# Performance work log

Measured on AMD Instinct MI355X. Metric: run time of the kernel, lower is better.

The kernel has to match this reference:

```python
import jax, jax.numpy as jnp
import numpy as np

B, L = 1024, 4096        # cycles x timesteps
CC = 3                   # SC channels (SC[...,2:3] = nominal capacity)
XC = 2 + CC              # p_net input: [SOC, T, SC...]
# bounds from params['a123'] for (R_1, 1/R_1C_1, OCV-U, -M_H, K_H)
LB = jnp.array([0.005, 0.025, 0.1, 0.0, 0.002], dtype=jnp.float32)
UB = jnp.array([0.02, 0.07, 1.0, 0.055, 0.025], dtype=jnp.float32)


def setup_inputs() -> dict:
    key = jax.random.key(0)
    ks = jax.random.split(key, 10)
    t = jnp.broadcast_to(jnp.arange(L, dtype=jnp.float32), (B, L))  # monotone time
    I = 1.0 + 0.1 * jax.random.normal(ks[0], (B, L))  # current, bounded away from 0 (IR_estim divides by I)
    T = jax.random.normal(ks[1], (B, L))              # temperature
    dummy = jax.random.normal(ks[2], (B, L))          # unused column 3
    SOC = jax.random.uniform(ks[3], (B, L))
    X = jnp.stack([t, I, T, dummy, SOC], axis=-1)     # [B, L, 5]
    SC = jax.random.uniform(ks[4], (B, CC), minval=0.5, maxval=1.5)
    std = 0.1  # init_network_weights: normal(0, 0.1), zero bias
    pW1 = std * jax.random.normal(ks[5], (XC, 2 * XC))
    pb1 = jnp.zeros((2 * XC,), jnp.float32)
    pW2 = std * jax.random.normal(ks[6], (2 * XC, 5))
    pb2 = jnp.zeros((5,), jnp.float32)
    rW1 = std * jax.random.normal(ks[7], (XC, 1))
    rb1 = jnp.zeros((1,), jnp.float32)
    rW2 = std * jax.random.normal(ks[8], (1, 1))
    rb2 = jnp.zeros((1,), jnp.float32)
    return dict(X=X, SC=SC, pW1=pW1, pb1=pb1, pW2=pW2, pb2=pb2,
                rW1=rW1, rb1=rb1, rW2=rW2, rb2=rb2)


def reference(X, SC, pW1, pb1, pW2, pb2, rW1, rb1, rW2, rb2):
    t = X[..., 0:1]
    I = X[..., 1:2]
    T = X[..., 2:3]
    SOC = X[..., 4:]
    sc_b = jnp.broadcast_to(SC[:, None, :], (X.shape[0], X.shape[1], SC.shape[-1]))
    x = jnp.concatenate([SOC, T, sc_b], axis=-1)                 # [B, L, XC]
    p = jax.nn.softplus(x @ pW1 + pb1) @ pW2 + pb2               # [B, L, 5]
    theta = LB + (UB - LB) * jax.nn.sigmoid(0.01 * p)
    R_1 = theta[..., 0:1]
    RC_r = theta[..., 1:2]
    OCV_U = theta[..., 2:3]
    M_Hn = theta[..., 3:4]   # -M_H
    K_H = theta[..., 4:5]
    r = jax.nn.softplus(x[:, 0, :] @ rW1 + rb1) @ rW2 + rb2      # [B, 1]
    R_s_init = SC[..., 2:3] * (1.0 + r)
    U_H0 = jnp.zeros((X.shape[0], 1), X.dtype)
    U_10 = -OCV_U[:, 0, :] - U_H0 - I[:, 0, :] * R_s_init
    y0 = jnp.concatenate([U_H0, U_10], axis=-1)                  # [B, 2]

    dt = jnp.swapaxes(t[:, 1:, :] - t[:, :-1, :], 0, 1)          # [L-1, B, 1]
    tm = lambda a: jnp.swapaxes(a[:, :-1, :], 0, 1)              # step inputs use X_ode[:, i]
    scan_in = (dt, tm(I), tm(R_1), tm(RC_r), tm(M_Hn), tm(K_H))

    def step(y, inp):  # explicit Euler, IRODEFunc derivative
        dt_i, I_i, R1_i, RC_i, MH_i, KH_i = inp
        U_H = y[..., 0:1]
        U_1 = y[..., 1:2]
        dU_H = -KH_i * I_i * (-MH_i - U_H)
        dU_1 = RC_i * (R1_i * I_i - U_1)
        y = y + dt_i * jnp.concatenate([dU_H, dU_1], axis=-1)
        return y, y

    _, ys = jax.lax.scan(step, y0, scan_in)                      # [L-1, B, 2]
    voltages = jnp.concatenate([y0[None], ys], axis=0)           # [L, B, 2]
    voltages = jnp.swapaxes(voltages, 0, 1)                      # [B, L, 2]
    U_H = voltages[..., 0:1]
    U_1 = voltages[..., 1:2]
    IR_estim = jnp.nanmean((-OCV_U - U_H - U_1) / I, axis=-2)    # [B, 1]
    return IR_estim
```

## Files before the change

kernel.cpp:

```cpp
#include <hip/hip_runtime.h>

#define NB   1024
#define NL   4096
#define TPB  256
#define QSTEP 1024
#define SPT  4

#define WS_PART 16640

typedef float v2f __attribute__((ext_vector_type(2)));

__device__ __forceinline__ float fast_rcp(float x) { return __builtin_amdgcn_rcpf(x); }
__device__ __forceinline__ float fexp2(float x) { return __builtin_amdgcn_exp2f(x); }
__device__ __forceinline__ float flog2(float x) { return __builtin_amdgcn_logf(x); }

#define L2E 1.44269504088896340736f
#define LN2 0.69314718055994530942f

#define SP_C0 1.0f
#define SP_C1 0.0864667f
#define SP_C2 (-0.0015685f)
#define SP_C3 2.5763e-5f

__global__ void __launch_bounds__(TPB) onenet_main(
    const float* __restrict__ X,   const float* __restrict__ SC,
    const float* __restrict__ pW1, const float* __restrict__ pb1,
    const float* __restrict__ pW2, const float* __restrict__ pb2,
    const float* __restrict__ rW1, const float* __restrict__ rb1,
    const float* __restrict__ rW2, const float* __restrict__ rb2,
    float* __restrict__ ws)
{
    __shared__ float4 tile[TPB * 5];
    __shared__ float  red[TPB / 64][9];

    const int bid  = blockIdx.x;
    const int row  = bid >> 2;
    const int q    = bid & 3;
    const int tid  = threadIdx.x;
    const int lane = tid & 63;
    const int w    = tid >> 6;

    const float* Xq = X + ((size_t)row * NL + (size_t)q * QSTEP) * 5;
    {
        const float4* gq = (const float4*)Xq;
#pragma unroll
        for (int k = 0; k < 5; ++k) {
            int widx = tid + TPB * k;
            int sw   = widx ^ ((widx >> 3) & 7);
            tile[sw] = gq[widx];
        }
    }

    const float sc0 = SC[row * 3 + 0];
    const float sc1 = SC[row * 3 + 1];
    const float sc2 = SC[row * 3 + 2];

    float W1S[10], W1T[10], BASE[10];
    float VR1[10], VRC[10], VOC[10], VMH[10], VKH[10];
#pragma unroll
    for (int j = 0; j < 10; ++j) {
        W1S[j]  = L2E * pW1[j];
        W1T[j]  = L2E * pW1[10 + j];
        BASE[j] = L2E * fmaf(sc0, pW1[20 + j],
                        fmaf(sc1, pW1[30 + j],
                        fmaf(sc2, pW1[40 + j], pb1[j])));
    }
    const float UBLB0 = 0.015f, UBLB1 = 0.045f, UBLB2 = 0.9f,
                UBLB3 = 0.055f, UBLB4 = 0.023f;
    const float KC = LN2 * 0.0025f;
#pragma unroll
    for (int j = 0; j < 10; ++j) {
        VR1[j] = KC * UBLB0 * pW2[5 * j + 0];
        VRC[j] = KC * UBLB1 * pW2[5 * j + 1];
        VOC[j] = KC * UBLB2 * pW2[5 * j + 2];
        VMH[j] = KC * UBLB3 * pW2[5 * j + 3];
        VKH[j] = KC * UBLB4 * pW2[5 * j + 4];
    }
    const float A0 = 0.005f + UBLB0 * fmaf(0.0025f, pb2[0], 0.5f);
    const float A1 = 0.025f + UBLB1 * fmaf(0.0025f, pb2[1], 0.5f);
    const float A2 = 0.1f   + UBLB2 * fmaf(0.0025f, pb2[2], 0.5f);
    const float A3 = 0.0f   + UBLB3 * fmaf(0.0025f, pb2[3], 0.5f);
    const float A4 = 0.002f + UBLB4 * fmaf(0.0025f, pb2[4], 0.5f);

    float Rs = 0.f;
    if (q == 0) {
        const float* x0 = X + (size_t)row * NL * 5;
        float T0 = x0[2], SOC0 = x0[4];
        float u = rb1[0];
        u = fmaf(SOC0, rW1[0], u);
        u = fmaf(T0,   rW1[1], u);
        u = fmaf(sc0,  rW1[2], u);
        u = fmaf(sc1,  rW1[3], u);
        u = fmaf(sc2,  rW1[4], u);
        float sp = LN2 * flog2(1.0f + fexp2(L2E * u));
        Rs = sc2 * (1.0f + fmaf(sp, rW2[0], rb2[0]));
    }

    __syncthreads();

    float f[20];
#pragma unroll
    for (int j = 0; j < 5; ++j) {
        int widx = 5 * tid + j;
        int sw   = widx ^ ((widx >> 3) & 7);
        *(float4*)&f[4 * j] = tile[sw];
    }
    float tn;
    {
        int wn  = 5 * ((tid + 1) & (TPB - 1));
        int swn = wn ^ ((wn >> 3) & 7);
        float tl = tile[swn].x;
        if (tid < TPB - 1)      tn = tl;
        else if (q == 3)        tn = f[15];
        else                    tn = Xq[QSTEP * 5];
    }

    v2f a = {1.f, 1.f}, b = {0.f, 0.f}, cS = {0.f, 0.f}, dS = {0.f, 0.f};
    v2f oaccv = {0.f, 0.f};
    float OCV0 = 0.f, I0 = 0.f;

#pragma unroll
    for (int ip = 0; ip < 2; ++ip) {
        const int i0 = 2 * ip, i1 = 2 * ip + 1;
        v2f SSv = { f[5 * i0 + 4], f[5 * i1 + 4] };
        v2f Ttv = { f[5 * i0 + 2], f[5 * i1 + 2] };
        v2f Iv  = { f[5 * i0 + 1], f[5 * i1 + 1] };
        float tnx1 = (i1 < SPT - 1) ? f[5 * i1 + 5] : tn;
        v2f dtv = { f[5 * i1 + 0] - f[5 * i0 + 0], tnx1 - f[5 * i1 + 0] };
        v2f invv = { fast_rcp(Iv.x), fast_rcp(Iv.y) };

        v2f tR1 = {A0, A0}, tRC = {A1, A1}, tOC = {A2, A2},
            tMH = {A3, A3}, tKH = {A4, A4};
#pragma unroll
        for (int j = 0; j < 10; ++j) {
            v2f pre = SSv * W1S[j] + Ttv * W1T[j] + BASE[j];
            v2f s   = pre * pre;
            v2f p   = s * SP_C3 + SP_C2;
            p = s * p + SP_C1;
            p = s * p + SP_C0;
            v2f lam = pre * 0.5f + p;
            tR1 += lam * VR1[j];
            tRC += lam * VRC[j];
            tOC += lam * VOC[j];
            tMH += lam * VMH[j];
            tKH += lam * VKH[j];
        }
        oaccv += tOC * invv;
        if (ip == 0) { OCV0 = tOC.x; I0 = Iv.x; }

        v2f g  = dtv * tKH * Iv;
        v2f hh = dtv * tRC;
        v2f bx = g * tMH;
        v2f by = hh * tR1 * Iv;

        {
            v2f sv = {1.f + g.x, 1.f - hh.x};
            v2f bv = {bx.x, by.x};
            v2f iv = {invv.x, invv.x};
            cS = iv * a + cS;
            dS = iv * b + dS;
            b  = sv * b + bv;
            a  = sv * a;
        }
        {
            v2f sv = {1.f + g.y, 1.f - hh.y};
            v2f bv = {bx.y, by.y};
            v2f iv = {invv.y, invv.y};
            cS = iv * a + cS;
            dS = iv * b + dS;
            b  = sv * b + bv;
            a  = sv * a;
        }
    }
    float oacc = -(oaccv.x + oaccv.y);

#pragma unroll
    for (int off = 1; off < 64; off <<= 1) {
        v2f a2, b2, c2, d2;
        a2.x = __shfl_down(a.x, off);  a2.y = __shfl_down(a.y, off);
        b2.x = __shfl_down(b.x, off);  b2.y = __shfl_down(b.y, off);
        c2.x = __shfl_down(cS.x, off); c2.y = __shfl_down(cS.y, off);
        d2.x = __shfl_down(dS.x, off); d2.y = __shfl_down(dS.y, off);
        float o2 = __shfl_down(oacc, off);
        v2f nb = a2 * b + b2;
        v2f nc = c2 * a + cS;
        v2f nd = (dS + d2) + c2 * b;
        a = a2 * a; b = nb; cS = nc; dS = nd;
        oacc += o2;
    }

    if (lane == 0) {
        red[w][0] = a.x;  red[w][1] = a.y;
        red[w][2] = b.x;  red[w][3] = b.y;
        red[w][4] = cS.x; red[w][5] = cS.y;
        red[w][6] = dS.x; red[w][7] = dS.y;
        red[w][8] = oacc;
    }
    __syncthreads();

    if (tid == 0) {
#pragma unroll
        for (int k = 1; k < TPB / 64; ++k) {
            v2f ak, bk, ck, dk;
            ak.x = red[k][0]; ak.y = red[k][1];
            bk.x = red[k][2]; bk.y = red[k][3];
            ck.x = red[k][4]; ck.y = red[k][5];
            dk.x = red[k][6]; dk.y = red[k][7];
            v2f nb = ak * b + bk;
            v2f nc = ck * a + cS;
            v2f nd = (dS + dk) + ck * b;
            a = ak * a; b = nb; cS = nc; dS = nd;
            oacc += red[k][8];
        }
        float* pw = ws + WS_PART + (size_t)bid * 12;
        pw[0] = a.x;  pw[1] = b.x;  pw[2] = cS.x; pw[3] = dS.x;
        pw[4] = a.y;  pw[5] = b.y;  pw[6] = cS.y; pw[7] = dS.y;
        pw[8] = oacc;
        if (q == 0) { pw[9] = OCV0; pw[10] = I0; pw[11] = Rs; }
    }
}

__global__ void __launch_bounds__(256) onenet_final(
    const float* __restrict__ ws, float* __restrict__ out)
{
    const int row = blockIdx.x * 256 + threadIdx.x;
    if (row >= NB) return;
    const float* p0 = ws + WS_PART + (size_t)row * 48;

    v2f a, b, cS, dS;
    a.x  = p0[0]; a.y  = p0[4];
    b.x  = p0[1]; b.y  = p0[5];
    cS.x = p0[2]; cS.y = p0[6];
    dS.x = p0[3]; dS.y = p0[7];
    float O = p0[8];
    float OCV0 = p0[9], I0 = p0[10], Rs = p0[11];
#pragma unroll
    for (int k = 1; k < 4; ++k) {
        const float* pk = p0 + k * 12;
        v2f ak, bk, ck, dk;
        ak.x = pk[0]; ak.y = pk[4];
        bk.x = pk[1]; bk.y = pk[5];
        ck.x = pk[2]; ck.y = pk[6];
        dk.x = pk[3]; dk.y = pk[7];
        v2f nb = ak * b + bk;
        v2f nc = ck * a + cS;
        v2f nd = (dS + dk) + ck * b;
        a = ak * a; b = nb; cS = nc; dS = nd;
        O += pk[8];
    }
    float U10 = -OCV0 - I0 * Rs;
    float SH  = dS.x;
    float S1  = fmaf(cS.y, U10, dS.y);
    out[row] = (O - SH - S1) * (1.0f / 4096.0f);
}

extern "C" void kernel_launch(void* const* d_in, const int* in_sizes, int n_in,
                              void* d_out, int out_size, void* d_ws, size_t ws_size,
                              hipStream_t stream) {
    const float* X   = (const float*)d_in[0];
    const float* SC  = (const float*)d_in[1];
    const float* pW1 = (const float*)d_in[2];
    const float* pb1 = (const float*)d_in[3];
    const float* pW2 = (const float*)d_in[4];
    const float* pb2 = (const float*)d_in[5];
    const float* rW1 = (const float*)d_in[6];
    const float* rb1 = (const float*)d_in[7];
    const float* rW2 = (const float*)d_in[8];
    const float* rb2 = (const float*)d_in[9];
    float* out = (float*)d_out;
    float* ws  = (float*)d_ws;

    onenet_main<<<NB * 4, TPB, 0, stream>>>(X, SC, pW1, pb1, pW2, pb2,
                                            rW1, rb1, rW2, rb2, ws);
    onenet_final<<<NB / 256, 256, 0, stream>>>(ws, out);
}
```

Baseline: 141.7 us.

## Fuse main and final kernels with one block per row and direct-to-LDS loads

Each row is now handled by a single 256-thread block that processes 16 timesteps per thread in four chunks. This removes the second reduction kernel and the workspace round-trip. The full 80 KB row tile is loaded with global_load_lds straight into shared memory, replacing the register-staged loads. The large LDS footprint cuts occupancy to about one block per CU, and the grid shrinks from 4096 blocks to 1024, which limits latency hiding.

```diff
diff --git a/kernel.cpp b/kernel.cpp
--- a/kernel.cpp
+++ b/kernel.cpp
@@ -3,10 +3,7 @@
 #define NB   1024
 #define NL   4096
 #define TPB  256
-#define QSTEP 1024
-#define SPT  4
-
-#define WS_PART 16640
+#define NCH  4
 
 typedef float v2f __attribute__((ext_vector_type(2)));
 
@@ -22,33 +19,32 @@
 #define SP_C2 (-0.0015685f)
 #define SP_C3 2.5763e-5f
 
-__global__ void __launch_bounds__(TPB) onenet_main(
+__global__ void __launch_bounds__(TPB) onenet_fused(
     const float* __restrict__ X,   const float* __restrict__ SC,
     const float* __restrict__ pW1, const float* __restrict__ pb1,
     const float* __restrict__ pW2, const float* __restrict__ pb2,
     const float* __restrict__ rW1, const float* __restrict__ rb1,
     const float* __restrict__ rW2, const float* __restrict__ rb2,
-    float* __restrict__ ws)
+    float* __restrict__ out)
 {
-    __shared__ float4 tile[TPB * 5];
-    __shared__ float  red[TPB / 64][9];
-
-    const int bid  = blockIdx.x;
-    const int row  = bid >> 2;
-    const int q    = bid & 3;
+    __shared__ float4 tile[5120];
+
+    const int row  = blockIdx.x;
     const int tid  = threadIdx.x;
     const int lane = tid & 63;
     const int w    = tid >> 6;
 
-    const float* Xq = X + ((size_t)row * NL + (size_t)q * QSTEP) * 5;
-    {
-        const float4* gq = (const float4*)Xq;
-#pragma unroll
-        for (int k = 0; k < 5; ++k) {
-            int widx = tid + TPB * k;
-            int sw   = widx ^ ((widx >> 3) & 7);
-            tile[sw] = gq[widx];
-        }
+    const float* Xrow = X + (size_t)row * NL * 5;
+
+#pragma unroll
+    for (int k = 0; k < 20; ++k) {
+        int jbase = 256 * k + 64 * w;
+        int j     = jbase + lane;
+        int sj    = j ^ ((j >> 3) & 7);
+        __builtin_amdgcn_global_load_lds(
+            (const __attribute__((address_space(1))) void*)(Xrow + 4 * (size_t)sj),
+            (__attribute__((address_space(3))) void*)&tile[jbase],
+            16, 0, 0);
     }
 
     const float sc0 = SC[row * 3 + 0];
@@ -82,10 +78,9 @@
     const float A3 = 0.0f   + UBLB3 * fmaf(0.0025f, pb2[3], 0.5f);
     const float A4 = 0.002f + UBLB4 * fmaf(0.0025f, pb2[4], 0.5f);
 
-    float Rs = 0.f;
-    if (q == 0) {
-        const float* x0 = X + (size_t)row * NL * 5;
-        float T0 = x0[2], SOC0 = x0[4];
+    float Rs;
+    {
+        float T0 = Xrow[2], SOC0 = Xrow[4];
         float u = rb1[0];
         u = fmaf(SOC0, rW1[0], u);
         u = fmaf(T0,   rW1[1], u);
@@ -98,78 +93,83 @@
 
     __syncthreads();
 
-    float f[20];
-#pragma unroll
-    for (int j = 0; j < 5; ++j) {
-        int widx = 5 * tid + j;
-        int sw   = widx ^ ((widx >> 3) & 7);
-        *(float4*)&f[4 * j] = tile[sw];
-    }
-    float tn;
-    {
-        int wn  = 5 * ((tid + 1) & (TPB - 1));
-        int swn = wn ^ ((wn >> 3) & 7);
-        float tl = tile[swn].x;
-        if (tid < TPB - 1)      tn = tl;
-        else if (q == 3)        tn = f[15];
-        else                    tn = Xq[QSTEP * 5];
-    }
-
     v2f a = {1.f, 1.f}, b = {0.f, 0.f}, cS = {0.f, 0.f}, dS = {0.f, 0.f};
     v2f oaccv = {0.f, 0.f};
     float OCV0 = 0.f, I0 = 0.f;
-
-#pragma unroll
-    for (int ip = 0; ip < 2; ++ip) {
-        const int i0 = 2 * ip, i1 = 2 * ip + 1;
-        v2f SSv = { f[5 * i0 + 4], f[5 * i1 + 4] };
-        v2f Ttv = { f[5 * i0 + 2], f[5 * i1 + 2] };
-        v2f Iv  = { f[5 * i0 + 1], f[5 * i1 + 1] };
-        float tnx1 = (i1 < SPT - 1) ? f[5 * i1 + 5] : tn;
-        v2f dtv = { f[5 * i1 + 0] - f[5 * i0 + 0], tnx1 - f[5 * i1 + 0] };
-        v2f invv = { fast_rcp(Iv.x), fast_rcp(Iv.y) };
-
-        v2f tR1 = {A0, A0}, tRC = {A1, A1}, tOC = {A2, A2},
-            tMH = {A3, A3}, tKH = {A4, A4};
-#pragma unroll
-        for (int j = 0; j < 10; ++j) {
-            v2f pre = SSv * W1S[j] + Ttv * W1T[j] + BASE[j];
-            v2f s   = pre * pre;
-            v2f p   = s * SP_C3 + SP_C2;
-            p = s * p + SP_C1;
-            p = s * p + SP_C0;
-            v2f lam = pre * 0.5f + p;
-            tR1 += lam * VR1[j];
-            tRC += lam * VRC[j];
-            tOC += lam * VOC[j];
-            tMH += lam * VMH[j];
-            tKH += lam * VKH[j];
-        }
-        oaccv += tOC * invv;
-        if (ip == 0) { OCV0 = tOC.x; I0 = Iv.x; }
-
-        v2f g  = dtv * tKH * Iv;
-        v2f hh = dtv * tRC;
-        v2f bx = g * tMH;
-        v2f by = hh * tR1 * Iv;
-
+    const float* tf = (const float*)tile;
+
+#pragma unroll
+    for (int c = 0; c < NCH; ++c) {
+        float f[20];
+#pragma unroll
+        for (int jj = 0; jj < 5; ++jj) {
+            int i4 = 20 * tid + 5 * c + jj;
+            int s4 = i4 ^ ((i4 >> 3) & 7);
+            *(float4*)&f[4 * jj] = tile[s4];
+        }
+        float tn;
         {
-            v2f sv = {1.f + g.x, 1.f - hh.x};
-            v2f bv = {bx.x, by.x};
-            v2f iv = {invv.x, invv.x};
-            cS = iv * a + cS;
-            dS = iv * b + dS;
-            b  = sv * b + bv;
-            a  = sv * a;
-        }
-        {
-            v2f sv = {1.f + g.y, 1.f - hh.y};
-            v2f bv = {bx.y, by.y};
-            v2f iv = {invv.y, invv.y};
-            cS = iv * a + cS;
-            dS = iv * b + dS;
-            b  = sv * b + bv;
-            a  = sv * a;
+            int i4 = 20 * tid + 5 * c + 5;
+            if (i4 < 5120) {
+                int s4 = i4 ^ ((i4 >> 3) & 7);
+                tn = tf[4 * s4];
+            } else {
+                tn = f[15];
+            }
+        }
+
+#pragma unroll
+        for (int ip = 0; ip < 2; ++ip) {
+            const int i0 = 2 * ip, i1 = 2 * ip + 1;
+            v2f SSv = { f[5 * i0 + 4], f[5 * i1 + 4] };
+            v2f Ttv = { f[5 * i0 + 2], f[5 * i1 + 2] };
+            v2f Iv  = { f[5 * i0 + 1], f[5 * i1 + 1] };
+            float tnx1 = (ip == 0) ? f[5 * i1 + 5] : tn;
+            v2f dtv = { f[5 * i1 + 0] - f[5 * i0 + 0], tnx1 - f[5 * i1 + 0] };
+            v2f invv = { fast_rcp(Iv.x), fast_rcp(Iv.y) };
+
+            v2f tR1 = {A0, A0}, tRC = {A1, A1}, tOC = {A2, A2},
+                tMH = {A3, A3}, tKH = {A4, A4};
+#pragma unroll
+            for (int j = 0; j < 10; ++j) {
+                v2f pre = SSv * W1S[j] + Ttv * W1T[j] + BASE[j];
+                v2f s   = pre * pre;
+                v2f p   = s * SP_C3 + SP_C2;
+                p = s * p + SP_C1;
+                p = s * p + SP_C0;
+                v2f lam = pre * 0.5f + p;
+                tR1 += lam * VR1[j];
+                tRC += lam * VRC[j];
+                tOC += lam * VOC[j];
+                tMH += lam * VMH[j];
+                tKH += lam * VKH[j];
+            }
+            oaccv += tOC * invv;
+            if (c == 0 && ip == 0) { OCV0 = tOC.x; I0 = Iv.x; }
+
+            v2f g  = dtv * tKH * Iv;
+            v2f hh = dtv * tRC;
+            v2f bx = g * tMH;
+            v2f by = hh * tR1 * Iv;
+
+            {
+                v2f sv = {1.f + g.x, 1.f - hh.x};
+                v2f bv = {bx.x, by.x};
+                v2f iv = {invv.x, invv.x};
+                cS = iv * a + cS;
+                dS = iv * b + dS;
+                b  = sv * b + bv;
+                a  = sv * a;
+            }
+            {
+                v2f sv = {1.f + g.y, 1.f - hh.y};
+                v2f bv = {bx.y, by.y};
+                v2f iv = {invv.y, invv.y};
+                cS = iv * a + cS;
+                dS = iv * b + dS;
+                b  = sv * b + bv;
+                a  = sv * a;
+            }
         }
     }
     float oacc = -(oaccv.x + oaccv.y);
@@ -189,12 +189,14 @@
         oacc += o2;
     }
 
+    __syncthreads();
+    float* redf = (float*)tile;
     if (lane == 0) {
-        red[w][0] = a.x;  red[w][1] = a.y;
-        red[w][2] = b.x;  red[w][3] = b.y;
-        red[w][4] = cS.x; red[w][5] = cS.y;
-        red[w][6] = dS.x; red[w][7] = dS.y;
-        red[w][8] = oacc;
+        redf[w * 12 + 0] = a.x;  redf[w * 12 + 1] = a.y;
+        redf[w * 12 + 2] = b.x;  redf[w * 12 + 3] = b.y;
+        redf[w * 12 + 4] = cS.x; redf[w * 12 + 5] = cS.y;
+        redf[w * 12 + 6] = dS.x; redf[w * 12 + 7] = dS.y;
+        redf[w * 12 + 8] = oacc;
     }
     __syncthreads();
 
@@ -202,56 +204,21 @@
 #pragma unroll
         for (int k = 1; k < TPB / 64; ++k) {
             v2f ak, bk, ck, dk;
-            ak.x = red[k][0]; ak.y = red[k][1];
-            bk.x = red[k][2]; bk.y = red[k][3];
-            ck.x = red[k][4]; ck.y = red[k][5];
-            dk.x = red[k][6]; dk.y = red[k][7];
+            ak.x = redf[k * 12 + 0]; ak.y = redf[k * 12 + 1];
+            bk.x = redf[k * 12 + 2]; bk.y = redf[k * 12 + 3];
+            ck.x = redf[k * 12 + 4]; ck.y = redf[k * 12 + 5];
+            dk.x = redf[k * 12 + 6]; dk.y = redf[k * 12 + 7];
             v2f nb = ak * b + bk;
             v2f nc = ck * a + cS;
             v2f nd = (dS + dk) + ck * b;
             a = ak * a; b = nb; cS = nc; dS = nd;
-            oacc += red[k][8];
-        }
-        float* pw = ws + WS_PART + (size_t)bid * 12;
-        pw[0] = a.x;  pw[1] = b.x;  pw[2] = cS.x; pw[3] = dS.x;
-        pw[4] = a.y;  pw[5] = b.y;  pw[6] = cS.y; pw[7] = dS.y;
-        pw[8] = oacc;
-        if (q == 0) { pw[9] = OCV0; pw[10] = I0; pw[11] = Rs; }
-    }
-}
-
-__global__ void __launch_bounds__(256) onenet_final(
-    const float* __restrict__ ws, float* __restrict__ out)
-{
-    const int row = blockIdx.x * 256 + threadIdx.x;
-    if (row >= NB) return;
-    const float* p0 = ws + WS_PART + (size_t)row * 48;
-
-    v2f a, b, cS, dS;
-    a.x  = p0[0]; a.y  = p0[4];
-    b.x  = p0[1]; b.y  = p0[5];
-    cS.x = p0[2]; cS.y = p0[6];
-    dS.x = p0[3]; dS.y = p0[7];
-    float O = p0[8];
-    float OCV0 = p0[9], I0 = p0[10], Rs = p0[11];
-#pragma unroll
-    for (int k = 1; k < 4; ++k) {
-        const float* pk = p0 + k * 12;
-        v2f ak, bk, ck, dk;
-        ak.x = pk[0]; ak.y = pk[4];
-        bk.x = pk[1]; bk.y = pk[5];
-        ck.x = pk[2]; ck.y = pk[6];
-        dk.x = pk[3]; dk.y = pk[7];
-        v2f nb = ak * b + bk;
-        v2f nc = ck * a + cS;
-        v2f nd = (dS + dk) + ck * b;
-        a = ak * a; b = nb; cS = nc; dS = nd;
-        O += pk[8];
-    }
-    float U10 = -OCV0 - I0 * Rs;
-    float SH  = dS.x;
-    float S1  = fmaf(cS.y, U10, dS.y);
-    out[row] = (O - SH - S1) * (1.0f / 4096.0f);
+            oacc += redf[k * 12 + 8];
+        }
+        float U10 = -OCV0 - I0 * Rs;
+        float SH  = dS.x;
+        float S1  = fmaf(cS.y, U10, dS.y);
+        out[row] = (oacc - SH - S1) * (1.0f / 4096.0f);
+    }
 }
 
 extern "C" void kernel_launch(void* const* d_in, const int* in_sizes, int n_in,
@@ -268,9 +235,8 @@
     const float* rW2 = (const float*)d_in[8];
     const float* rb2 = (const float*)d_in[9];
     float* out = (float*)d_out;
-    float* ws  = (float*)d_ws;
-
-    onenet_main<<<NB * 4, TPB, 0, stream>>>(X, SC, pW1, pb1, pW2, pb2,
-                                            rW1, rb1, rW2, rb2, ws);
-    onenet_final<<<NB / 256, 256, 0, stream>>>(ws, out);
+    (void)d_ws; (void)ws_size;
+
+    onenet_fused<<<NB, TPB, 0, stream>>>(X, SC, pW1, pb1, pW2, pb2,
+                                         rW1, rb1, rW2, rb2, out);
 }
```

Result: slower. 152.9 us (+7.9%).

## Precompute per-row constants in prep kernel, fuse final reduce via atomic counter

Applied to the files above, without the earlier changes.

Adds a small prep kernel that computes the per-row first-layer bias terms, the initial resistance and the folded network constants into the workspace, and zeroes per-row counters. The main kernel reads these precomputed values instead of redoing them in every block, loads X directly into LDS with global_load_lds, and performs the final cross-quarter combine in the last-arriving block using an atomic counter and thread fences. This removes the separate final kernel and redundant per-block setup arithmetic. In exchange it adds a prep launch, atomics and fence overhead, and makes correctness depend on the counter reset and on memory ordering.

```diff
diff --git a/kernel.cpp b/kernel.cpp
--- a/kernel.cpp
+++ b/kernel.cpp
@@ -6,7 +6,9 @@
 #define QSTEP 1024
 #define SPT  4
 
+#define WS_BASE 256
 #define WS_PART 16640
+#define WS_CNT  65792
 
 typedef float v2f __attribute__((ext_vector_type(2)));
 
@@ -22,7 +24,7 @@
 #define SP_C2 (-0.0015685f)
 #define SP_C3 2.5763e-5f
 
-__global__ void __launch_bounds__(TPB) onenet_main(
+__global__ void __launch_bounds__(256) onenet_prep(
     const float* __restrict__ X,   const float* __restrict__ SC,
     const float* __restrict__ pW1, const float* __restrict__ pb1,
     const float* __restrict__ pW2, const float* __restrict__ pb2,
@@ -30,61 +32,19 @@
     const float* __restrict__ rW2, const float* __restrict__ rb2,
     float* __restrict__ ws)
 {
-    __shared__ float4 tile[TPB * 5];
-    __shared__ float  red[TPB / 64][9];
-
-    const int bid  = blockIdx.x;
-    const int row  = bid >> 2;
-    const int q    = bid & 3;
-    const int tid  = threadIdx.x;
-    const int lane = tid & 63;
-    const int w    = tid >> 6;
-
-    const float* Xq = X + ((size_t)row * NL + (size_t)q * QSTEP) * 5;
-    {
-        const float4* gq = (const float4*)Xq;
-#pragma unroll
-        for (int k = 0; k < 5; ++k) {
-            int widx = tid + TPB * k;
-            int sw   = widx ^ ((widx >> 3) & 7);
-            tile[sw] = gq[widx];
-        }
-    }
-
-    const float sc0 = SC[row * 3 + 0];
-    const float sc1 = SC[row * 3 + 1];
-    const float sc2 = SC[row * 3 + 2];
-
-    float W1S[10], W1T[10], BASE[10];
-    float VR1[10], VRC[10], VOC[10], VMH[10], VKH[10];
-#pragma unroll
-    for (int j = 0; j < 10; ++j) {
-        W1S[j]  = L2E * pW1[j];
-        W1T[j]  = L2E * pW1[10 + j];
-        BASE[j] = L2E * fmaf(sc0, pW1[20 + j],
-                        fmaf(sc1, pW1[30 + j],
-                        fmaf(sc2, pW1[40 + j], pb1[j])));
-    }
-    const float UBLB0 = 0.015f, UBLB1 = 0.045f, UBLB2 = 0.9f,
-                UBLB3 = 0.055f, UBLB4 = 0.023f;
-    const float KC = LN2 * 0.0025f;
-#pragma unroll
-    for (int j = 0; j < 10; ++j) {
-        VR1[j] = KC * UBLB0 * pW2[5 * j + 0];
-        VRC[j] = KC * UBLB1 * pW2[5 * j + 1];
-        VOC[j] = KC * UBLB2 * pW2[5 * j + 2];
-        VMH[j] = KC * UBLB3 * pW2[5 * j + 3];
-        VKH[j] = KC * UBLB4 * pW2[5 * j + 4];
-    }
-    const float A0 = 0.005f + UBLB0 * fmaf(0.0025f, pb2[0], 0.5f);
-    const float A1 = 0.025f + UBLB1 * fmaf(0.0025f, pb2[1], 0.5f);
-    const float A2 = 0.1f   + UBLB2 * fmaf(0.0025f, pb2[2], 0.5f);
-    const float A3 = 0.0f   + UBLB3 * fmaf(0.0025f, pb2[3], 0.5f);
-    const float A4 = 0.002f + UBLB4 * fmaf(0.0025f, pb2[4], 0.5f);
-
-    float Rs = 0.f;
-    if (q == 0) {
-        const float* x0 = X + (size_t)row * NL * 5;
+    const int gid = blockIdx.x * 256 + threadIdx.x;
+    if (gid < NB) {
+        ((unsigned*)ws)[WS_CNT + gid] = 0u;
+        float sc0 = SC[gid * 3 + 0], sc1 = SC[gid * 3 + 1], sc2 = SC[gid * 3 + 2];
+        float* bp = ws + WS_BASE + gid * 16;
+#pragma unroll
+        for (int j = 0; j < 10; ++j) {
+            float base = fmaf(sc0, pW1[20 + j],
+                         fmaf(sc1, pW1[30 + j],
+                         fmaf(sc2, pW1[40 + j], pb1[j])));
+            bp[j] = L2E * base;
+        }
+        const float* x0 = X + (size_t)gid * NL * 5;
         float T0 = x0[2], SOC0 = x0[4];
         float u = rb1[0];
         u = fmaf(SOC0, rW1[0], u);
@@ -93,17 +53,82 @@
         u = fmaf(sc1,  rW1[3], u);
         u = fmaf(sc2,  rW1[4], u);
         float sp = LN2 * flog2(1.0f + fexp2(L2E * u));
-        Rs = sc2 * (1.0f + fmaf(sp, rW2[0], rb2[0]));
+        float r  = fmaf(sp, rW2[0], rb2[0]);
+        bp[10] = sc2 * (1.0f + r);
+    }
+    if (blockIdx.x == 0 && threadIdx.x < 75) {
+        const int t = threadIdx.x;
+        const float LBv[5]   = {0.005f, 0.025f, 0.1f, 0.0f, 0.002f};
+        const float UBLB[5]  = {0.015f, 0.045f, 0.9f, 0.055f, 0.023f};
+        float v;
+        if (t < 20) {
+            v = L2E * pW1[t];
+        } else if (t < 70) {
+            int k = (t - 20) % 5;
+            v = LN2 * 0.0025f * UBLB[k] * pW2[t - 20];
+        } else {
+            int k = t - 70;
+            v = LBv[k] + UBLB[k] * fmaf(0.0025f, pb2[k], 0.5f);
+        }
+        ws[t] = v;
+    }
+}
+
+__global__ void __launch_bounds__(TPB) onenet_main(
+    const float* __restrict__ X, float* __restrict__ ws,
+    float* __restrict__ out)
+{
+    __shared__ float4 tile[TPB * 5];
+    __shared__ float  red[TPB / 64][9];
+
+    const int bid  = blockIdx.x;
+    const int row  = bid >> 2;
+    const int q    = bid & 3;
+    const int tid  = threadIdx.x;
+    const int lane = tid & 63;
+    const int w    = tid >> 6;
+
+    const float* Xq = X + ((size_t)row * NL + (size_t)q * QSTEP) * 5;
+#pragma unroll
+    for (int k = 0; k < 5; ++k) {
+        int jbase = 320 * w + 64 * k;
+        int j     = jbase + lane;
+        int sj    = j ^ ((j >> 3) & 7);
+        __builtin_amdgcn_global_load_lds(
+            (const __attribute__((address_space(1))) void*)(Xq + 4 * (size_t)sj),
+            (__attribute__((address_space(3))) void*)&tile[jbase],
+            16, 0, 0);
+    }
+
+    float W1S[10], W1T[10], BASE[10];
+    float VR1[10], VRC[10], VOC[10], VMH[10], VKH[10];
+#pragma unroll
+    for (int j = 0; j < 10; ++j) W1S[j] = ws[j];
+#pragma unroll
+    for (int j = 0; j < 10; ++j) W1T[j] = ws[10 + j];
+#pragma unroll
+    for (int j = 0; j < 10; ++j) {
+        VR1[j] = ws[20 + 5 * j + 0];
+        VRC[j] = ws[20 + 5 * j + 1];
+        VOC[j] = ws[20 + 5 * j + 2];
+        VMH[j] = ws[20 + 5 * j + 3];
+        VKH[j] = ws[20 + 5 * j + 4];
+    }
+    const float A0 = ws[70], A1 = ws[71], A2 = ws[72], A3 = ws[73], A4 = ws[74];
+    {
+        const float* bp = ws + WS_BASE + row * 16;
+#pragma unroll
+        for (int j = 0; j < 10; ++j) BASE[j] = bp[j];
     }
 
     __syncthreads();
 
     float f[20];
 #pragma unroll
-    for (int j = 0; j < 5; ++j) {
-        int widx = 5 * tid + j;
+    for (int jj = 0; jj < 5; ++jj) {
+        int widx = 5 * tid + jj;
         int sw   = widx ^ ((widx >> 3) & 7);
-        *(float4*)&f[4 * j] = tile[sw];
+        *(float4*)&f[4 * jj] = tile[sw];
     }
     float tn;
     {
@@ -125,7 +150,7 @@
         v2f SSv = { f[5 * i0 + 4], f[5 * i1 + 4] };
         v2f Ttv = { f[5 * i0 + 2], f[5 * i1 + 2] };
         v2f Iv  = { f[5 * i0 + 1], f[5 * i1 + 1] };
-        float tnx1 = (i1 < SPT - 1) ? f[5 * i1 + 5] : tn;
+        float tnx1 = (ip == 0) ? f[5 * i1 + 5] : tn;
         v2f dtv = { f[5 * i1 + 0] - f[5 * i0 + 0], tnx1 - f[5 * i1 + 0] };
         v2f invv = { fast_rcp(Iv.x), fast_rcp(Iv.y) };
 
@@ -216,42 +241,41 @@
         pw[0] = a.x;  pw[1] = b.x;  pw[2] = cS.x; pw[3] = dS.x;
         pw[4] = a.y;  pw[5] = b.y;  pw[6] = cS.y; pw[7] = dS.y;
         pw[8] = oacc;
-        if (q == 0) { pw[9] = OCV0; pw[10] = I0; pw[11] = Rs; }
-    }
-}
-
-__global__ void __launch_bounds__(256) onenet_final(
-    const float* __restrict__ ws, float* __restrict__ out)
-{
-    const int row = blockIdx.x * 256 + threadIdx.x;
-    if (row >= NB) return;
-    const float* p0 = ws + WS_PART + (size_t)row * 48;
-
-    v2f a, b, cS, dS;
-    a.x  = p0[0]; a.y  = p0[4];
-    b.x  = p0[1]; b.y  = p0[5];
-    cS.x = p0[2]; cS.y = p0[6];
-    dS.x = p0[3]; dS.y = p0[7];
-    float O = p0[8];
-    float OCV0 = p0[9], I0 = p0[10], Rs = p0[11];
-#pragma unroll
-    for (int k = 1; k < 4; ++k) {
-        const float* pk = p0 + k * 12;
-        v2f ak, bk, ck, dk;
-        ak.x = pk[0]; ak.y = pk[4];
-        bk.x = pk[1]; bk.y = pk[5];
-        ck.x = pk[2]; ck.y = pk[6];
-        dk.x = pk[3]; dk.y = pk[7];
-        v2f nb = ak * b + bk;
-        v2f nc = ck * a + cS;
-        v2f nd = (dS + dk) + ck * b;
-        a = ak * a; b = nb; cS = nc; dS = nd;
-        O += pk[8];
-    }
-    float U10 = -OCV0 - I0 * Rs;
-    float SH  = dS.x;
-    float S1  = fmaf(cS.y, U10, dS.y);
-    out[row] = (O - SH - S1) * (1.0f / 4096.0f);
+        if (q == 0) { pw[9] = OCV0; pw[10] = I0; }
+
+        __threadfence();
+        unsigned old = atomicAdd(((unsigned*)ws) + WS_CNT + row, 1u);
+        if (old == 3u) {
+            __threadfence();
+            const float* p0 = ws + WS_PART + (size_t)row * 48;
+            v2f A_, B_, C_, D_;
+            A_.x = p0[0]; A_.y = p0[4];
+            B_.x = p0[1]; B_.y = p0[5];
+            C_.x = p0[2]; C_.y = p0[6];
+            D_.x = p0[3]; D_.y = p0[7];
+            float O = p0[8];
+            float OCV00 = p0[9], I00 = p0[10];
+#pragma unroll
+            for (int k = 1; k < 4; ++k) {
+                const float* pk = p0 + k * 12;
+                v2f ak, bk, ck, dk;
+                ak.x = pk[0]; ak.y = pk[4];
+                bk.x = pk[1]; bk.y = pk[5];
+                ck.x = pk[2]; ck.y = pk[6];
+                dk.x = pk[3]; dk.y = pk[7];
+                v2f nb = ak * B_ + bk;
+                v2f nc = ck * A_ + C_;
+                v2f nd = (D_ + dk) + ck * B_;
+                A_ = ak * A_; B_ = nb; C_ = nc; D_ = nd;
+                O += pk[8];
+            }
+            float Rs  = ws[WS_BASE + row * 16 + 10];
+            float U10 = -OCV00 - I00 * Rs;
+            float SH  = D_.x;
+            float S1  = fmaf(C_.y, U10, D_.y);
+            out[row] = (O - SH - S1) * (1.0f / 4096.0f);
+        }
+    }
 }
 
 extern "C" void kernel_launch(void* const* d_in, const int* in_sizes, int n_in,
@@ -270,7 +294,7 @@
     float* out = (float*)d_out;
     float* ws  = (float*)d_ws;
 
-    onenet_main<<<NB * 4, TPB, 0, stream>>>(X, SC, pW1, pb1, pW2, pb2,
-                                            rW1, rb1, rW2, rb2, ws);
-    onenet_final<<<NB / 256, 256, 0, stream>>>(ws, out);
+    onenet_prep<<<NB / 256, 256, 0, stream>>>(X, SC, pW1, pb1, pW2, pb2,
+                                              rW1, rb1, rW2, rb2, ws);
+    onenet_main<<<NB * 4, TPB, 0, stream>>>(X, ws, out);
 }
```

Result: slower. 371.9 us (+162.5%).
